# Kernel optimization log

Hardware: AMD Instinct MI355X
Metric: run time of the kernel (lower is better)

Reference implementation:

```python
import jax, jax.numpy as jnp
import numpy as np

jax.config.update("jax_enable_x64", True)

NNZ = 8_388_608        # number of sparse (feature_id, value) pairs
N_FEATURES = 8_192     # number of calibrated feature ids
N_BIN = 63             # bin boundaries per feature -> 64 bins
OUT_BITS = 22          # output id space = 1 << 22
GOLDEN32 = np.uint32(0x9E3779B9)  # Knuth multiplicative-hashing constant


def setup_inputs() -> dict:
    key = jax.random.key(0)
    k1, k2, k3 = jax.random.split(key, 3)
    input_keys = jax.random.randint(k1, (NNZ,), 0, 2 * N_FEATURES, dtype=jnp.int64)
    input_vals = jax.random.normal(k2, (NNZ,), dtype=jnp.float32)
    # Calibrated feature ids (sorted) and per-feature sorted bin boundaries.
    feature_ids = jnp.arange(N_FEATURES, dtype=jnp.int64)
    bin_vals = jnp.sort(
        jax.random.normal(k3, (N_FEATURES, N_BIN), dtype=jnp.float32), axis=1
    ).reshape(-1)
    return {
        "input_keys": input_keys,
        "input_vals": input_vals,
        "feature_ids": feature_ids,
        "bin_vals": bin_vals,
    }


def _lower_bound_bins(bin_vals_flat, feat_idx, vals, n_bin):
    """Per-value branchless binary search: bin = sum(bin_row < val).

    bin_vals_flat: [F * n_bin] row-sorted boundaries, feat_idx: [nnz] int,
    vals: [nnz] float. Returns [nnz] int32 bin index in [0, n_bin].
    """
    steps = int(np.ceil(np.log2(n_bin + 1)))  # 6 for n_bin=63
    base = feat_idx.astype(jnp.int64) * n_bin
    lo = jnp.zeros(vals.shape, dtype=jnp.int32)
    hi = jnp.full(vals.shape, n_bin, dtype=jnp.int32)
    for _ in range(steps):
        mid = (lo + hi) >> 1                       # in [0, n_bin]
        mid_safe = jnp.minimum(mid, n_bin - 1)     # gather-safe
        bv = bin_vals_flat[base + mid_safe]
        valid = lo < hi
        go_right = valid & (bv < vals)             # strict '<' => lower bound
        lo = jnp.where(go_right, mid + 1, lo)
        hi = jnp.where(valid & ~go_right, mid, hi)
    return lo


def reference(input_keys, input_vals, feature_ids, bin_vals):
    F = feature_ids.shape[0]
    n_bin = bin_vals.shape[0] // F
    mask = jnp.int64((1 << OUT_BITS) - 1)

    # --- find each key in the (sorted) calibrated feature-id table ---
    idx = jnp.searchsorted(feature_ids, input_keys)          # [nnz]
    idx_safe = jnp.minimum(idx, F - 1)
    calibrated = feature_ids[idx_safe] == input_keys          # [nnz] bool

    # --- bin assignment: bin = sum(bin_vals_row < val) ---
    bins = _lower_bound_bins(bin_vals, idx_safe, input_vals, n_bin)

    # --- 32-bit integer multiplicative hash of (feature_id, bin) ---
    h = (input_keys.astype(jnp.uint32) * GOLDEN32 + bins.astype(jnp.uint32)) * GOLDEN32
    hashed_key = h.astype(jnp.int64) & mask

    out_keys = jnp.where(calibrated, hashed_key, input_keys & mask)
    out_vals = jnp.where(calibrated, jnp.ones_like(input_vals), input_vals)
    # dense_shape of the resulting SparseTensor is [batch, 1 << OUT_BITS]
    return out_keys, out_vals
```

## Files before the change

kernel.cpp:

```cpp
#include <hip/hip_runtime.h>
#include <stdint.h>
#include <math.h>


#define GOLDEN   0x9E3779B9u
#define OUT_MASK ((1u << 22) - 1u)
#define NBIN  63
#define NPIV  8192
#define NKEY  16384

typedef float fx4 __attribute__((ext_vector_type(4)));
typedef int   ix4 __attribute__((ext_vector_type(4)));
typedef unsigned ux2 __attribute__((ext_vector_type(2)));

__device__ __forceinline__ unsigned bf16c(float x) {
    const unsigned b = __float_as_uint(x);
    unsigned t = ((int)b >= 0) ? ((b + 0xFFFFu) >> 16) : (b >> 16);
    return (t == 0x8000u) ? 0u : t;
}

__global__ __launch_bounds__(256) void build_tables_kernel(
    const int* __restrict__ fids, const float* __restrict__ bins,
    float* __restrict__ qtab, ux2* __restrict__ spiv8_g,
    unsigned char* __restrict__ scal_g, int F)
{
    const int t = blockIdx.x * blockDim.x + threadIdx.x;
    if (t >= F * 64) return;
    const int r = t >> 6;
    const int j = t & 63;
    const unsigned uk = (unsigned)fids[r];
    const float* src = bins + (size_t)r * NBIN;

    if (uk < (unsigned)NPIV) {
        qtab[((size_t)uk << 6) + j] = (j < NBIN) ? src[j] : INFINITY;
        if (j == 0) {
            const unsigned B15 = bf16c(src[15]);
            const unsigned B31 = bf16c(src[31]);
            const unsigned B47 = bf16c(src[47]);
            const unsigned tag = 0x6000u | uk;
            ux2 p;
            p.x = B15 | (B31 << 16);
            p.y = B47 | (tag << 16);
            spiv8_g[uk] = p;
        }
    } else if (uk < (unsigned)NKEY && j == 0) {
        scal_g[uk - NPIV] = (unsigned char)(0x40u | (uk & 63u));
    }
}

__device__ __forceinline__ void hd_fallback(
    int k, float v, const int* __restrict__ fids, const float* __restrict__ bins,
    int F, int fsteps, float& okey, float& oval)
{
    int lo = 0, hi = F;
    for (int s = 0; s < fsteps; ++s) {
        int  mid  = (lo + hi) >> 1;
        int  mids = min(mid, F - 1);
        int  fv   = fids[mids];
        bool valid = lo < hi;
        bool right = valid && (fv < k);
        lo = right ? mid + 1 : lo;
        hi = (valid && !right) ? mid : hi;
    }
    const int  idx_safe   = min(lo, F - 1);
    const bool calibrated = (fids[idx_safe] == k);
    const float* brow = bins + (size_t)idx_safe * NBIN;
    int blo = 0, bhi = NBIN;
    #pragma unroll
    for (int s = 0; s < 6; ++s) {
        int   mid  = (blo + bhi) >> 1;
        int   mids = min(mid, NBIN - 1);
        float bv   = brow[mids];
        bool  valid = blo < bhi;
        bool  right = valid && (bv < v);
        blo = right ? mid + 1 : blo;
        bhi = (valid && !right) ? mid : bhi;
    }
    const uint32_t h = ((uint32_t)k * GOLDEN + (uint32_t)blo) * GOLDEN;
    okey = calibrated ? (float)(h & OUT_MASK) : (float)((uint32_t)k & OUT_MASK);
    oval = calibrated ? 1.0f : v;
}

__device__ __forceinline__ int hd_cmp8(fx4 a, fx4 b, float v) {
    return (a.x < v) + (a.y < v) + (a.z < v) + (a.w < v)
         + (b.x < v) + (b.y < v) + (b.z < v) + (b.w < v);
}

__device__ __forceinline__ int hd_quad_bin(const char* qb, unsigned u,
                                           float v, int q)
{
    for (;;) {
        const char* p = qb + ((u << 8) + (unsigned)(q << 6));
        const fx4 a = *reinterpret_cast<const fx4*>(p);
        const fx4 b = *reinterpret_cast<const fx4*>(p + 16);
        const fx4 c = *reinterpret_cast<const fx4*>(p + 32);
        const fx4 d = *reinterpret_cast<const fx4*>(p + 48);
        const int cnt = hd_cmp8(a, b, v) + hd_cmp8(c, d, v);
        if (__builtin_expect(cnt == 16 && q < 3, 0)) { ++q; continue; }
        return (q << 4) + cnt;
    }
}

__global__ __launch_bounds__(1024, 8) void hd_main_kernel(
    const int* __restrict__ keys, const float* __restrict__ vals,
    const int* __restrict__ fids, const float* __restrict__ bins,
    const float* __restrict__ qtab, const ux2* __restrict__ spiv8_g,
    const unsigned char* __restrict__ scal_g,
    float* __restrict__ out_keys, float* __restrict__ out_vals,
    int n, int F, int fsteps, int nchunks)
{
    extern __shared__ char smem[];
    ux2*      spiv8 = reinterpret_cast<ux2*>(smem);
    unsigned* scal  = reinterpret_cast<unsigned*>(smem + (size_t)NPIV * 8);

    const int tid = threadIdx.x;
    for (int i = tid; i < NPIV; i += (int)blockDim.x) spiv8[i] = spiv8_g[i];
    const unsigned* scal_g32 = reinterpret_cast<const unsigned*>(scal_g);
    for (int i = tid; i < NPIV / 4; i += (int)blockDim.x) scal[i] = scal_g32[i];
    __syncthreads();

    const unsigned char* scal_b = reinterpret_cast<const unsigned char*>(scal);
    const char* qb = reinterpret_cast<const char*>(qtab);
    const int nthreads = (int)(gridDim.x * blockDim.x);

    for (int c = blockIdx.x * blockDim.x + tid; c < nchunks; c += nthreads) {
        const int i0 = c * 4;
        int   k0, k1, k2, k3;
        float v0, v1, v2, v3;
        const bool full = (i0 + 3 < n);
        if (full) {
            const ix4 ka = __builtin_nontemporal_load(reinterpret_cast<const ix4*>(keys + i0));
            const fx4 va = __builtin_nontemporal_load(reinterpret_cast<const fx4*>(vals + i0));
            k0 = ka.x; k1 = ka.y; k2 = ka.z; k3 = ka.w;
            v0 = va.x; v1 = va.y; v2 = va.z; v3 = va.w;
        } else {
            k0 = keys[min(i0 + 0, n - 1)]; v0 = vals[min(i0 + 0, n - 1)];
            k1 = keys[min(i0 + 1, n - 1)]; v1 = vals[min(i0 + 1, n - 1)];
            k2 = keys[min(i0 + 2, n - 1)]; v2 = vals[min(i0 + 2, n - 1)];
            k3 = keys[min(i0 + 3, n - 1)]; v3 = vals[min(i0 + 3, n - 1)];
        }

        const unsigned u0 = (unsigned)k0, u1 = (unsigned)k1,
                       u2 = (unsigned)k2, u3 = (unsigned)k3;

        const ux2 h0 = spiv8[u0 < (unsigned)NPIV ? u0 : 0u];
        const ux2 h1 = spiv8[u1 < (unsigned)NPIV ? u1 : 0u];
        const ux2 h2 = spiv8[u2 < (unsigned)NPIV ? u2 : 0u];
        const ux2 h3 = spiv8[u3 < (unsigned)NPIV ? u3 : 0u];

#define HD_BF(B) __uint_as_float((B) << 16)
#define HD_P2(J)                                                              \
        const bool cal##J = (u##J < (unsigned)NPIV) &&                        \
                            ((h##J.y >> 16) == (0x6000u | u##J));             \
        const int q##J = (HD_BF(h##J.x & 0xFFFFu) < v##J)                     \
                       + (HD_BF(h##J.x >> 16)     < v##J)                     \
                       + (HD_BF(h##J.y & 0xFFFFu) < v##J);                    \
        const unsigned hs##J = u##J - (unsigned)NPIV;                         \
        const bool rare##J =                                                  \
            (u##J >= (unsigned)NKEY) ||                                       \
            ((hs##J < (unsigned)NPIV) &&                                      \
             (scal_b[hs##J < (unsigned)NPIV ? hs##J : 0u] ==                  \
              (unsigned char)(0x40u | (u##J & 63u))));
        HD_P2(0) HD_P2(1) HD_P2(2) HD_P2(3)
#undef HD_P2
#undef HD_BF

        float ok0, ok1, ok2, ok3, ov0, ov1, ov2, ov3;
#define HD_P3(J)                                                              \
        if (cal##J) {                                                         \
            const int bin = hd_quad_bin(qb, u##J, v##J, q##J);                \
            const uint32_t h = (u##J * GOLDEN + (uint32_t)bin) * GOLDEN;      \
            ok##J = (float)(h & OUT_MASK);                                    \
            ov##J = 1.0f;                                                     \
        } else {                                                              \
            ok##J = (float)(u##J & OUT_MASK);                                 \
            ov##J = v##J;                                                     \
        }
        HD_P3(0) HD_P3(1) HD_P3(2) HD_P3(3)
#undef HD_P3

        if (__builtin_expect(rare0 | rare1 | rare2 | rare3, 0)) {
            if (rare0) hd_fallback(k0, v0, fids, bins, F, fsteps, ok0, ov0);
            if (rare1) hd_fallback(k1, v1, fids, bins, F, fsteps, ok1, ov1);
            if (rare2) hd_fallback(k2, v2, fids, bins, F, fsteps, ok2, ov2);
            if (rare3) hd_fallback(k3, v3, fids, bins, F, fsteps, ok3, ov3);
        }

        if (full) {
            fx4 s;
            s.x = ok0; s.y = ok1; s.z = ok2; s.w = ok3;
            __builtin_nontemporal_store(s, reinterpret_cast<fx4*>(out_keys + i0));
            s.x = ov0; s.y = ov1; s.z = ov2; s.w = ov3;
            __builtin_nontemporal_store(s, reinterpret_cast<fx4*>(out_vals + i0));
        } else {
            if (i0 + 0 < n) { out_keys[i0 + 0] = ok0; out_vals[i0 + 0] = ov0; }
            if (i0 + 1 < n) { out_keys[i0 + 1] = ok1; out_vals[i0 + 1] = ov1; }
            if (i0 + 2 < n) { out_keys[i0 + 2] = ok2; out_vals[i0 + 2] = ov2; }
            if (i0 + 3 < n) { out_keys[i0 + 3] = ok3; out_vals[i0 + 3] = ov3; }
        }
    }
}

__global__ __launch_bounds__(256) void hd_simple_kernel(
    const int* __restrict__ keys, const float* __restrict__ vals,
    const int* __restrict__ fids, const float* __restrict__ bins,
    float* __restrict__ out_keys, float* __restrict__ out_vals,
    int n, int F, int fsteps)
{
    const int gid = blockIdx.x * blockDim.x + threadIdx.x;
    const int i0 = gid * 4;
    if (i0 >= n) return;
    #pragma unroll
    for (int j = 0; j < 4; ++j) {
        int idx = min(i0 + j, n - 1);
        float okey, oval;
        hd_fallback(keys[idx], vals[idx], fids, bins, F, fsteps, okey, oval);
        if (i0 + j < n) { out_keys[i0 + j] = okey; out_vals[i0 + j] = oval; }
    }
}

extern "C" void kernel_launch(void* const* d_in, const int* in_sizes, int n_in,
                              void* d_out, int out_size, void* d_ws, size_t ws_size,
                              hipStream_t stream) {
    const int*   keys = (const int*)d_in[0];
    const float* vals = (const float*)d_in[1];
    const int*   fids = (const int*)d_in[2];
    const float* bins = (const float*)d_in[3];

    const int n = in_sizes[0];
    const int F = in_sizes[2];

    int fsteps = 0;
    while ((1 << fsteps) < F + 1) ++fsteps;

    float* out_keys = (float*)d_out;
    float* out_vals = (float*)d_out + n;

    const size_t qtab_bytes = (size_t)NPIV * 64 * sizeof(float);
    const size_t spiv_bytes = (size_t)NPIV * 8;
    const size_t scal_bytes = (size_t)NPIV;
    const size_t ws_need    = qtab_bytes + spiv_bytes + scal_bytes;
    const size_t lds_bytes  = spiv_bytes + scal_bytes;

    int max_lds = 0;
    hipDeviceGetAttribute(&max_lds, hipDeviceAttributeMaxSharedMemoryPerBlock, 0);

    const bool fast = (ws_size >= ws_need) && ((size_t)max_lds >= lds_bytes) &&
                      (in_sizes[3] == F * NBIN) && (F <= NPIV);

    if (fast) {
        float*         qtab    = (float*)d_ws;
        ux2*           spiv8_g = (ux2*)((char*)d_ws + qtab_bytes);
        unsigned char* scal_g  = (unsigned char*)d_ws + qtab_bytes + spiv_bytes;

        build_tables_kernel<<<(F * 64 + 255) / 256, 256, 0, stream>>>(
            fids, bins, qtab, spiv8_g, scal_g, F);

        (void)hipFuncSetAttribute(
            reinterpret_cast<const void*>(hd_main_kernel),
            hipFuncAttributeMaxDynamicSharedMemorySize, (int)lds_bytes);

        const int threads = 1024;
        const int nblocks = 512;
        const int nchunks = (n + 3) / 4;
        hd_main_kernel<<<nblocks, threads, lds_bytes, stream>>>(
            keys, vals, fids, bins, qtab, spiv8_g, scal_g,
            out_keys, out_vals, n, F, fsteps, nchunks);
    } else {
        const int threads = 256;
        const int grid = (n + threads * 4 - 1) / (threads * 4);
        hd_simple_kernel<<<grid, threads, 0, stream>>>(
            keys, vals, fids, bins, out_keys, out_vals, n, F, fsteps);
    }
}
```

Before: 159.8 us.

## Widen LDS pivot table to seven bf16 pivots and scan 8-wide leaves

The per-feature LDS pivot record grows from 8 to 16 bytes and holds seven bf16 pivots instead of three. The first-level search therefore picks one of eight 8-element segments, so each lookup reads 32 bytes of the global bin table instead of 64, cutting gather traffic. In exchange LDS use per block doubles to about 136 KB, occupancy drops (launch bounds 1024,4) and the grid is halved to 256 blocks, with more ALU work spent on pivot compares.

Result: faster. 152.9 us (-4.3%).

```diff
diff --git a/kernel.cpp b/kernel.cpp
--- a/kernel.cpp
+++ b/kernel.cpp
@@ -11,7 +11,7 @@
 
 typedef float fx4 __attribute__((ext_vector_type(4)));
 typedef int   ix4 __attribute__((ext_vector_type(4)));
-typedef unsigned ux2 __attribute__((ext_vector_type(2)));
+typedef unsigned ux4 __attribute__((ext_vector_type(4)));
 
 __device__ __forceinline__ unsigned bf16c(float x) {
     const unsigned b = __float_as_uint(x);
@@ -21,7 +21,7 @@
 
 __global__ __launch_bounds__(256) void build_tables_kernel(
     const int* __restrict__ fids, const float* __restrict__ bins,
-    float* __restrict__ qtab, ux2* __restrict__ spiv8_g,
+    float* __restrict__ qtab, ux4* __restrict__ spiv16_g,
     unsigned char* __restrict__ scal_g, int F)
 {
     const int t = blockIdx.x * blockDim.x + threadIdx.x;
@@ -34,14 +34,17 @@
     if (uk < (unsigned)NPIV) {
         qtab[((size_t)uk << 6) + j] = (j < NBIN) ? src[j] : INFINITY;
         if (j == 0) {
-            const unsigned B15 = bf16c(src[15]);
-            const unsigned B31 = bf16c(src[31]);
-            const unsigned B47 = bf16c(src[47]);
+            const unsigned p0 = bf16c(src[7]),  p1 = bf16c(src[15]),
+                           p2 = bf16c(src[23]), p3 = bf16c(src[31]),
+                           p4 = bf16c(src[39]), p5 = bf16c(src[47]),
+                           p6 = bf16c(src[55]);
             const unsigned tag = 0x6000u | uk;
-            ux2 p;
-            p.x = B15 | (B31 << 16);
-            p.y = B47 | (tag << 16);
-            spiv8_g[uk] = p;
+            ux4 q;
+            q.x = p0 | (p1 << 16);
+            q.y = p2 | (p3 << 16);
+            q.z = p4 | (p5 << 16);
+            q.w = p6 | (tag << 16);
+            spiv16_g[uk] = q;
         }
     } else if (uk < (unsigned)NKEY && j == 0) {
         scal_g[uk - NPIV] = (unsigned char)(0x40u | (uk & 63u));
@@ -86,35 +89,33 @@
          + (b.x < v) + (b.y < v) + (b.z < v) + (b.w < v);
 }
 
-__device__ __forceinline__ int hd_quad_bin(const char* qb, unsigned u,
-                                           float v, int q)
+__device__ __forceinline__ int hd_leaf_bin(const char* qb, unsigned u,
+                                           float v, int t)
 {
     for (;;) {
-        const char* p = qb + ((u << 8) + (unsigned)(q << 6));
+        const char* p = qb + ((u << 8) + (unsigned)(t << 5));
         const fx4 a = *reinterpret_cast<const fx4*>(p);
         const fx4 b = *reinterpret_cast<const fx4*>(p + 16);
-        const fx4 c = *reinterpret_cast<const fx4*>(p + 32);
-        const fx4 d = *reinterpret_cast<const fx4*>(p + 48);
-        const int cnt = hd_cmp8(a, b, v) + hd_cmp8(c, d, v);
-        if (__builtin_expect(cnt == 16 && q < 3, 0)) { ++q; continue; }
-        return (q << 4) + cnt;
-    }
-}
-
-__global__ __launch_bounds__(1024, 8) void hd_main_kernel(
+        const int cnt = hd_cmp8(a, b, v);
+        if (__builtin_expect(cnt == 8 && t < 7, 0)) { ++t; continue; }
+        return (t << 3) + cnt;
+    }
+}
+
+__global__ __launch_bounds__(1024, 4) void hd_main_kernel(
     const int* __restrict__ keys, const float* __restrict__ vals,
     const int* __restrict__ fids, const float* __restrict__ bins,
-    const float* __restrict__ qtab, const ux2* __restrict__ spiv8_g,
+    const float* __restrict__ qtab, const ux4* __restrict__ spiv16_g,
     const unsigned char* __restrict__ scal_g,
     float* __restrict__ out_keys, float* __restrict__ out_vals,
     int n, int F, int fsteps, int nchunks)
 {
     extern __shared__ char smem[];
-    ux2*      spiv8 = reinterpret_cast<ux2*>(smem);
-    unsigned* scal  = reinterpret_cast<unsigned*>(smem + (size_t)NPIV * 8);
+    ux4*      spiv16 = reinterpret_cast<ux4*>(smem);
+    unsigned* scal   = reinterpret_cast<unsigned*>(smem + (size_t)NPIV * 16);
 
     const int tid = threadIdx.x;
-    for (int i = tid; i < NPIV; i += (int)blockDim.x) spiv8[i] = spiv8_g[i];
+    for (int i = tid; i < NPIV; i += (int)blockDim.x) spiv16[i] = spiv16_g[i];
     const unsigned* scal_g32 = reinterpret_cast<const unsigned*>(scal_g);
     for (int i = tid; i < NPIV / 4; i += (int)blockDim.x) scal[i] = scal_g32[i];
     __syncthreads();
@@ -143,18 +144,22 @@
         const unsigned u0 = (unsigned)k0, u1 = (unsigned)k1,
                        u2 = (unsigned)k2, u3 = (unsigned)k3;
 
-        const ux2 h0 = spiv8[u0 < (unsigned)NPIV ? u0 : 0u];
-        const ux2 h1 = spiv8[u1 < (unsigned)NPIV ? u1 : 0u];
-        const ux2 h2 = spiv8[u2 < (unsigned)NPIV ? u2 : 0u];
-        const ux2 h3 = spiv8[u3 < (unsigned)NPIV ? u3 : 0u];
+        const ux4 h0 = spiv16[u0 < (unsigned)NPIV ? u0 : 0u];
+        const ux4 h1 = spiv16[u1 < (unsigned)NPIV ? u1 : 0u];
+        const ux4 h2 = spiv16[u2 < (unsigned)NPIV ? u2 : 0u];
+        const ux4 h3 = spiv16[u3 < (unsigned)NPIV ? u3 : 0u];
 
 #define HD_BF(B) __uint_as_float((B) << 16)
 #define HD_P2(J)                                                              \
         const bool cal##J = (u##J < (unsigned)NPIV) &&                        \
-                            ((h##J.y >> 16) == (0x6000u | u##J));             \
-        const int q##J = (HD_BF(h##J.x & 0xFFFFu) < v##J)                     \
+                            ((h##J.w >> 16) == (0x6000u | u##J));             \
+        const int t##J = (HD_BF(h##J.x & 0xFFFFu) < v##J)                     \
                        + (HD_BF(h##J.x >> 16)     < v##J)                     \
-                       + (HD_BF(h##J.y & 0xFFFFu) < v##J);                    \
+                       + (HD_BF(h##J.y & 0xFFFFu) < v##J)                     \
+                       + (HD_BF(h##J.y >> 16)     < v##J)                     \
+                       + (HD_BF(h##J.z & 0xFFFFu) < v##J)                     \
+                       + (HD_BF(h##J.z >> 16)     < v##J)                     \
+                       + (HD_BF(h##J.w & 0xFFFFu) < v##J);                    \
         const unsigned hs##J = u##J - (unsigned)NPIV;                         \
         const bool rare##J =                                                  \
             (u##J >= (unsigned)NKEY) ||                                       \
@@ -168,7 +173,7 @@
         float ok0, ok1, ok2, ok3, ov0, ov1, ov2, ov3;
 #define HD_P3(J)                                                              \
         if (cal##J) {                                                         \
-            const int bin = hd_quad_bin(qb, u##J, v##J, q##J);                \
+            const int bin = hd_leaf_bin(qb, u##J, v##J, t##J);                \
             const uint32_t h = (u##J * GOLDEN + (uint32_t)bin) * GOLDEN;      \
             ok##J = (float)(h & OUT_MASK);                                    \
             ov##J = 1.0f;                                                     \
@@ -237,7 +242,7 @@
     float* out_vals = (float*)d_out + n;
 
     const size_t qtab_bytes = (size_t)NPIV * 64 * sizeof(float);
-    const size_t spiv_bytes = (size_t)NPIV * 8;
+    const size_t spiv_bytes = (size_t)NPIV * 16;
     const size_t scal_bytes = (size_t)NPIV;
     const size_t ws_need    = qtab_bytes + spiv_bytes + scal_bytes;
     const size_t lds_bytes  = spiv_bytes + scal_bytes;
@@ -249,22 +254,22 @@
                       (in_sizes[3] == F * NBIN) && (F <= NPIV);
 
     if (fast) {
-        float*         qtab    = (float*)d_ws;
-        ux2*           spiv8_g = (ux2*)((char*)d_ws + qtab_bytes);
-        unsigned char* scal_g  = (unsigned char*)d_ws + qtab_bytes + spiv_bytes;
+        float*         qtab     = (float*)d_ws;
+        ux4*           spiv16_g = (ux4*)((char*)d_ws + qtab_bytes);
+        unsigned char* scal_g   = (unsigned char*)d_ws + qtab_bytes + spiv_bytes;
 
         build_tables_kernel<<<(F * 64 + 255) / 256, 256, 0, stream>>>(
-            fids, bins, qtab, spiv8_g, scal_g, F);
+            fids, bins, qtab, spiv16_g, scal_g, F);
 
         (void)hipFuncSetAttribute(
             reinterpret_cast<const void*>(hd_main_kernel),
             hipFuncAttributeMaxDynamicSharedMemorySize, (int)lds_bytes);
 
         const int threads = 1024;
-        const int nblocks = 512;
+        const int nblocks = 256;
         const int nchunks = (n + 3) / 4;
         hd_main_kernel<<<nblocks, threads, lds_bytes, stream>>>(
-            keys, vals, fids, bins, qtab, spiv8_g, scal_g,
+            keys, vals, fids, bins, qtab, spiv16_g, scal_g,
             out_keys, out_vals, n, F, fsteps, nchunks);
     } else {
         const int threads = 256;
```
